# Optimization experiments

Hardware: AMD Instinct MI355X
Metric: run time of the kernel (lower is better)

## Reference

```python
import jax, jax.numpy as jnp
import numpy as np

EMBED_DIM = 1024
HEAD_SIZE = 64
N_HEAD = 16
N_QUERY_GROUPS = 4
SEQ_LEN = 2048
BATCH = 8


def setup_inputs() -> dict:
    key = jax.random.key(0)
    ks = jax.random.split(key, 7)
    s = 1.0 / np.sqrt(EMBED_DIM)
    x = jax.random.normal(ks[0], (BATCH, SEQ_LEN, EMBED_DIM), dtype=jnp.float32)
    Wq = jax.random.uniform(ks[1], (EMBED_DIM, N_HEAD * HEAD_SIZE), jnp.float32, -s, s)
    bq = jax.random.uniform(ks[2], (N_HEAD * HEAD_SIZE,), jnp.float32, -s, s)
    Wk = jax.random.uniform(ks[3], (EMBED_DIM, N_QUERY_GROUPS * HEAD_SIZE), jnp.float32, -s, s)
    bk = jax.random.uniform(ks[4], (N_QUERY_GROUPS * HEAD_SIZE,), jnp.float32, -s, s)
    Wv = jax.random.uniform(ks[5], (EMBED_DIM, N_QUERY_GROUPS * HEAD_SIZE), jnp.float32, -s, s)
    bv = jax.random.uniform(ks[6], (N_QUERY_GROUPS * HEAD_SIZE,), jnp.float32, -s, s)
    return {"x": x, "Wq": Wq, "bq": bq, "Wk": Wk, "bk": bk, "Wv": Wv, "bv": bv}


def reference(x, Wq, bq, Wk, bk, Wv, bv):
    B, T, _ = x.shape
    rep = N_HEAD // N_QUERY_GROUPS  # queries per group
    Q = x @ Wq + bq  # (B, T, H*hs)
    # GQA: torch .repeat tiles the group-block [g0..g3, g0..g3, ...]
    K = (x @ Wk + bk).reshape(B, T, N_QUERY_GROUPS, HEAD_SIZE)
    K = jnp.tile(K, (1, 1, rep, 1)).reshape(B, T, N_HEAD * HEAD_SIZE)
    V = (x @ Wv + bv).reshape(B, T, N_QUERY_GROUPS, HEAD_SIZE)
    V = jnp.tile(V, (1, 1, rep, 1)).reshape(B, T, N_HEAD * HEAD_SIZE)
    # flattened-head scores: contract over full H*hs dim (as in source)
    att = jnp.einsum('btd,bsd->bts', Q, K)  # (B, T, T)
    causal = jnp.triu(jnp.ones((T, T), dtype=bool), k=1)
    mask = jnp.where(causal, jnp.float32(-jnp.inf), jnp.float32(0.0))[None, None]  # (1,1,T,T)
    att = att + mask  # broadcasts to (1, B, T, T), matching torch semantics
    att = jax.nn.softmax(att, axis=-1) / jnp.sqrt(jnp.float32(HEAD_SIZE))  # post-hoc scale, as in source
    out = jnp.einsum('xbts,bsd->xbtd', att, V)  # (1, B, T, H*hs)
    return out
```

## Files before the change

### kernel.cpp

```cpp
#include <hip/hip_runtime.h>
#include <float.h>
#include <stdint.h>

#define T_ 2048
#define DG 256

typedef _Float16 half8 __attribute__((ext_vector_type(8)));
typedef _Float16 half4v __attribute__((ext_vector_type(4)));
typedef __fp16 fp16x2 __attribute__((ext_vector_type(2)));
typedef float f32x4 __attribute__((ext_vector_type(4)));
typedef float f32x16 __attribute__((ext_vector_type(16)));
typedef unsigned uint2v __attribute__((ext_vector_type(2)));

#define PSTRIDE 8256

__device__ __forceinline__ void gload16(const void* g, void* l) {
  __builtin_amdgcn_global_load_lds(
      (const __attribute__((address_space(1))) unsigned int*)g,
      (__attribute__((address_space(3))) unsigned int*)l, 16, 0, 0);
}
#define WAIT_VMC(N)  do { asm volatile("s_waitcnt vmcnt(" #N ")" ::: "memory"); __builtin_amdgcn_sched_barrier(0); } while (0)
#define WAIT_LGKM0() do { asm volatile("s_waitcnt lgkmcnt(0)" ::: "memory"); __builtin_amdgcn_sched_barrier(0); } while (0)

__device__ __forceinline__ float cross32(float x, int g) {
  unsigned u = __builtin_bit_cast(unsigned, x);
  uint2v r = __builtin_amdgcn_permlane32_swap(u, u, false, false);
  return __builtin_bit_cast(float, g ? r[0] : r[1]);
}

__global__ __launch_bounds__(256) void prep_w(
    const float* __restrict__ Wq, const float* __restrict__ bq,
    const float* __restrict__ Wk, const float* __restrict__ bk,
    const float* __restrict__ Wv, const float* __restrict__ bv,
    _Float16* __restrict__ Wt, float* __restrict__ bcat) {
  for (int idx = blockIdx.x * 256 + threadIdx.x; idx < 786432; idx += 768 * 256) {
    int n = idx >> 10, k = idx & 1023;
    float v;
    if (n < 256)      v = Wq[k * 1024 + n] + Wq[k * 1024 + n + 256]
                        + Wq[k * 1024 + n + 512] + Wq[k * 1024 + n + 768];
    else if (n < 512) v = Wk[k * 256 + n - 256];
    else              v = Wv[k * 256 + n - 512];
    Wt[idx] = (_Float16)v;
    if (k == 0) {
      float bb;
      if (n < 256)      bb = bq[n] + bq[n + 256] + bq[n + 512] + bq[n + 768];
      else if (n < 512) bb = bk[n - 256];
      else              bb = bv[n - 512];
      bcat[n] = bb;
    }
  }
}

__global__ __launch_bounds__(256) void qkv_gemm(
    const float* __restrict__ x, const _Float16* __restrict__ Wt,
    const float* __restrict__ bcat,
    _Float16* __restrict__ Qh, _Float16* __restrict__ Kh, _Float16* __restrict__ Vf) {
  __shared__ __align__(16) uint8_t smem[65536];
  const int tid = threadIdx.x;
  const int w = tid >> 6, l = tid & 63;
  const int wr = w >> 1, wc = w & 1;
  const int lr = l & 15, lk = l >> 4;
  const int id = blockIdx.x;
  const int xcd = id & 7, s = id >> 3;
  const int m0 = (xcd + 8 * (s / 3)) * 128;
  const int by = s % 3;
  const int n0 = by * 256;

  f32x4 acc[4][8] = {};

  auto stage = [&](int k0, int buf) {
    uint8_t* Ab = smem + buf * 32768;
    uint8_t* Bb = Ab + 16384;
#pragma unroll
    for (int i = 0; i < 4; ++i) {
      int si = i * 256 + tid;
      int row = si >> 3, p = si & 7;
      gload16(x + (size_t)(m0 + row) * 1024 + k0 + ((p ^ (row & 7)) << 2), Ab + si * 16);
    }
#pragma unroll
    for (int i = 0; i < 4; ++i) {
      int si = i * 256 + tid;
      int row = si >> 2, p = si & 3;
      gload16(Wt + (size_t)(n0 + row) * 1024 + k0 + ((p ^ (row & 3)) << 3), Bb + si * 16);
    }
  };

  stage(0, 0);
  __syncthreads();

  for (int kt = 0; kt < 32; ++kt) {
    int cur = kt & 1;
    if (kt < 31) stage((kt + 1) * 32, cur ^ 1);
    const uint8_t* Ab = smem + cur * 32768;
    const uint8_t* Bb = Ab + 16384;
    half8 af[4], bf[8];
#pragma unroll
    for (int mi = 0; mi < 4; ++mi) {
      int row = wr * 64 + mi * 16 + lr;
      const float* pa = (const float*)(Ab + row * 128);
      f32x4 a0 = *(const f32x4*)(pa + ((((lk << 1))     ^ (row & 7)) << 2));
      f32x4 a1 = *(const f32x4*)(pa + ((((lk << 1) | 1) ^ (row & 7)) << 2));
      half8 h;
#pragma unroll
      for (int j = 0; j < 4; ++j) { h[j] = (_Float16)a0[j]; h[j + 4] = (_Float16)a1[j]; }
      af[mi] = h;
    }
#pragma unroll
    for (int ni = 0; ni < 8; ++ni) {
      int row = wc * 128 + ni * 16 + lr;
      bf[ni] = *(const half8*)(Bb + row * 64 + ((lk ^ (row & 3)) << 4));
    }
#pragma unroll
    for (int mi = 0; mi < 4; ++mi)
#pragma unroll
      for (int ni = 0; ni < 8; ++ni)
        acc[mi][ni] = __builtin_amdgcn_mfma_f32_16x16x32_f16(af[mi], bf[ni], acc[mi][ni], 0, 0, 0);
    __syncthreads();
  }

#pragma unroll
  for (int mi = 0; mi < 4; ++mi) {
#pragma unroll
    for (int ni = 0; ni < 8; ++ni) {
      int nl = wc * 128 + ni * 16 + lr;
      int mg = m0 + wr * 64 + mi * 16 + lk * 4;
      float bias = bcat[n0 + nl];
      if (by == 0) {
#pragma unroll
        for (int r = 0; r < 4; ++r)
          Qh[(size_t)(mg + r) * DG + nl] = (_Float16)((acc[mi][ni][r] + bias) * 1.44269504f);
      } else if (by == 1) {
#pragma unroll
        for (int r = 0; r < 4; ++r)
          Kh[(size_t)(mg + r) * DG + nl] = (_Float16)(acc[mi][ni][r] + bias);
      } else {
        int dt = nl >> 5, lnv = nl & 31;
        int bb = mg >> 11, t0 = mg & 2047;
        int st = t0 >> 5, sp = t0 & 31;
        int hs = sp >> 4, gg = (sp >> 3) & 1, j0 = sp & 7;
        size_t idx = (size_t)(((bb * 64 + st) * 8 + dt) * 2 + hs) * 512
                   + (gg * 32 + lnv) * 8 + j0;
        half4v h;
#pragma unroll
        for (int r = 0; r < 4; ++r) h[r] = (_Float16)(acc[mi][ni][r] + bias);
        *(half4v*)(Vf + idx) = h;
      }
    }
  }
}

__global__ __launch_bounds__(256, 3) void attn_main(
    const _Float16* __restrict__ Qg, const _Float16* __restrict__ Kg,
    const _Float16* __restrict__ Vf, float* __restrict__ out,
    float* __restrict__ partials) {
  __shared__ __align__(16) uint8_t smem[53248];
  const int tid = threadIdx.x;
  const int wv = tid >> 6;
  const int l  = tid & 63;
  const int g  = l >> 5;
  const int ln = l & 31;
  const int id = blockIdx.x;
  const int b  = id & 7;
  const int u  = id >> 3;
  int tt, c, nc;
  if (u < 64) { tt = 63 - (u >> 1); c = u & 1; nc = 2; }
  else        { tt = 95 - u;        c = 0;     nc = 1; }
  const int h  = (tt + 1) >> 1;
  const int lo = (nc == 2 && c == 1) ? h : 0;
  const int hi = (nc == 2 && c == 0) ? h : tt + 1;
  const int q0 = tt * 32;

  const _Float16* Kb  = Kg + (size_t)b * T_ * DG;
  const _Float16* Vfb = Vf + (size_t)b * 524288;
  float* Sx = (float*)(smem + 32768);

  const _Float16* Qrow = Qg + ((size_t)(b * T_ + q0 + ln)) * DG + wv * 64 + 8 * g;
  half8 qf[4];
#pragma unroll
  for (int j = 0; j < 4; ++j) qf[j] = *(const half8*)(Qrow + j * 16);

  f32x16 o0 = {}, o1 = {};
  float m_r = -1e30f, l_r = 0.0f;

  auto stageK = [&](int s0, int buf) {
    uint8_t* Kl = smem + buf * 16384;
#pragma unroll
    for (int i = 0; i < 4; ++i) {
      int si = i * 256 + tid;
      int row = si >> 5, part = si & 31;
      gload16(Kb + (size_t)(s0 + row) * DG + ((part ^ (row & 7)) << 3), Kl + si * 16);
    }
  };

  stageK(lo * 32, 0);
  WAIT_VMC(0);
  __builtin_amdgcn_s_barrier();

  for (int kt = lo; kt < hi; ++kt) {
    int cur = (kt - lo) & 1;
    const int dt0 = 2 * wv;
    half8 va0 = *(const half8*)(Vfb + (size_t)((kt * 8 + dt0) * 2 + 0) * 512 + l * 8);
    half8 va1 = *(const half8*)(Vfb + (size_t)((kt * 8 + dt0) * 2 + 1) * 512 + l * 8);
    half8 vb0 = *(const half8*)(Vfb + (size_t)((kt * 8 + dt0 + 1) * 2 + 0) * 512 + l * 8);
    half8 vb1 = *(const half8*)(Vfb + (size_t)((kt * 8 + dt0 + 1) * 2 + 1) * 512 + l * 8);

    const uint8_t* Klds = smem + cur * 16384;
    const int xr = (ln & 7) << 4;
    f32x16 s_acc = {};
    __builtin_amdgcn_s_setprio(1);
#pragma unroll
    for (int j = 0; j < 4; ++j) {
      half8 kf = *(const half8*)(Klds + ln * 512 + ((((4 * wv + j) * 32) + 16 * g) ^ xr));
      s_acc = __builtin_amdgcn_mfma_f32_32x32x16_f16(kf, qf[j], s_acc, 0, 0, 0);
    }
    __builtin_amdgcn_s_setprio(0);

    {
      float* myrow = Sx + (wv * 64 + l) * 20;
#pragma unroll
      for (int i = 0; i < 4; ++i)
        *(f32x4*)(myrow + 4 * i) = *(((const f32x4*)&s_acc) + i);
    }
    if (kt + 1 < hi) stageK((kt + 1) * 32, cur ^ 1);
    WAIT_LGKM0();
    __builtin_amdgcn_s_barrier();

    f32x4 sv[4];
#pragma unroll
    for (int i = 0; i < 4; ++i) sv[i] = *(((const f32x4*)&s_acc) + i);
#pragma unroll
    for (int wo = 0; wo < 4; ++wo) {
      if (wo == wv) continue;
      const float* prow = Sx + (wo * 64 + l) * 20;
#pragma unroll
      for (int i = 0; i < 4; ++i) sv[i] += *(const f32x4*)(prow + 4 * i);
    }
    float s[16];
#pragma unroll
    for (int r = 0; r < 16; ++r) s[r] = sv[r >> 2][r & 3];

    if (kt == tt) {
#pragma unroll
      for (int r = 0; r < 16; ++r) {
        int srow = (r & 3) + 8 * (r >> 2) + 4 * g;
        if (srow > ln) s[r] = -1e30f;
      }
    }
    float pmax = s[0];
#pragma unroll
    for (int r = 1; r < 16; ++r) pmax = fmaxf(pmax, s[r]);
    pmax = fmaxf(pmax, cross32(pmax, g));
    if (!__all(pmax <= m_r + 8.0f)) {
      float mnew = fmaxf(m_r, pmax);
      float sc = __builtin_amdgcn_exp2f(m_r - mnew);
      l_r *= sc;
#pragma unroll
      for (int r = 0; r < 16; ++r) { o0[r] *= sc; o1[r] *= sc; }
      m_r = mnew;
    }
    float p[16]; float psum = 0.0f;
#pragma unroll
    for (int r = 0; r < 16; ++r) { p[r] = __builtin_amdgcn_exp2f(s[r] - m_r); psum += p[r]; }
    l_r += psum + cross32(psum, g);

    unsigned ph[8];
#pragma unroll
    for (int i = 0; i < 8; ++i) {
      fp16x2 t2 = __builtin_amdgcn_cvt_pkrtz(p[2 * i], p[2 * i + 1]);
      ph[i] = __builtin_bit_cast(unsigned, t2);
    }
    union U { unsigned u[4]; half8 h; };
    U f0, f1;
    {
      uint2v r02 = __builtin_amdgcn_permlane32_swap(ph[0], ph[2], false, false);
      uint2v r13 = __builtin_amdgcn_permlane32_swap(ph[1], ph[3], false, false);
      uint2v r46 = __builtin_amdgcn_permlane32_swap(ph[4], ph[6], false, false);
      uint2v r57 = __builtin_amdgcn_permlane32_swap(ph[5], ph[7], false, false);
      f0.u[0] = r02[0]; f0.u[2] = r02[1];
      f0.u[1] = r13[0]; f0.u[3] = r13[1];
      f1.u[0] = r46[0]; f1.u[2] = r46[1];
      f1.u[1] = r57[0]; f1.u[3] = r57[1];
    }

    __builtin_amdgcn_s_setprio(1);
    o0 = __builtin_amdgcn_mfma_f32_32x32x16_f16(va0, f0.h, o0, 0, 0, 0);
    o0 = __builtin_amdgcn_mfma_f32_32x32x16_f16(va1, f1.h, o0, 0, 0, 0);
    o1 = __builtin_amdgcn_mfma_f32_32x32x16_f16(vb0, f0.h, o1, 0, 0, 0);
    o1 = __builtin_amdgcn_mfma_f32_32x32x16_f16(vb1, f1.h, o1, 0, 0, 0);
    __builtin_amdgcn_s_setprio(0);

    WAIT_VMC(0);
    __builtin_amdgcn_s_barrier();
  }

  float* chunk = (float*)(smem + wv * 4352);
  if (nc == 1) {
    float inv = 1.0f / (l_r * 8.0f);
    float* ob = out + ((size_t)(b * T_ + q0)) * 1024;
#pragma unroll
    for (int dtl = 0; dtl < 2; ++dtl) {
      const f32x16& oo = dtl ? o1 : o0;
      WAIT_LGKM0();
#pragma unroll
      for (int r = 0; r < 16; ++r) {
        int dl = (r & 3) + 8 * (r >> 2) + 4 * g;
        chunk[ln * 33 + dl] = oo[r] * inv;
      }
      WAIT_LGKM0();
#pragma unroll
      for (int rr = 0; rr < 2; ++rr) {
        int qq = (l >> 2) + 16 * rr;
        int cp = (l & 3) * 8;
        float vv[8];
#pragma unroll
        for (int jj = 0; jj < 8; ++jj) vv[jj] = chunk[qq * 33 + cp + jj];
        float4 w0 = make_float4(vv[0], vv[1], vv[2], vv[3]);
        float4 w1 = make_float4(vv[4], vv[5], vv[6], vv[7]);
        float* orow = ob + (size_t)qq * 1024 + (2 * wv + dtl) * 32 + cp;
#pragma unroll
        for (int rep = 0; rep < 4; ++rep) {
          *(float4*)(orow + rep * 256)     = w0;
          *(float4*)(orow + rep * 256 + 4) = w1;
        }
      }
    }
  } else {
    float* P = partials + (size_t)((b * 32 + (tt - 32)) * 2 + c) * PSTRIDE;
#pragma unroll
    for (int dtl = 0; dtl < 2; ++dtl) {
      const f32x16& oo = dtl ? o1 : o0;
      WAIT_LGKM0();
#pragma unroll
      for (int r = 0; r < 16; ++r) {
        int dl = (r & 3) + 8 * (r >> 2) + 4 * g;
        chunk[ln * 33 + dl] = oo[r];
      }
      WAIT_LGKM0();
#pragma unroll
      for (int rr = 0; rr < 2; ++rr) {
        int qq = (l >> 2) + 16 * rr;
        int cp = (l & 3) * 8;
        float vv[8];
#pragma unroll
        for (int jj = 0; jj < 8; ++jj) vv[jj] = chunk[qq * 33 + cp + jj];
        float* prow = P + qq * 256 + (2 * wv + dtl) * 32 + cp;
        *(float4*)prow       = make_float4(vv[0], vv[1], vv[2], vv[3]);
        *(float4*)(prow + 4) = make_float4(vv[4], vv[5], vv[6], vv[7]);
      }
    }
    if (wv == 0 && l < 32) { P[8192 + l] = m_r; P[8224 + l] = l_r; }
  }
}

__global__ __launch_bounds__(256) void attn_merge(
    const float* __restrict__ partials, float* __restrict__ out) {
  const int id = blockIdx.x;
  const int b = id & 7, tt = 32 + (id >> 3);
  const float* P0 = partials + (size_t)((b * 32 + (tt - 32)) * 2) * PSTRIDE;
  const float* P1 = P0 + PSTRIDE;
  const int tid = threadIdx.x;
  const int row = tid >> 3, cb = tid & 7;
  float m0 = P0[8192 + row], l0v = P0[8224 + row];
  float m1 = P1[8192 + row], l1v = P1[8224 + row];
  float M   = fmaxf(m0, m1);
  float sc0 = __builtin_amdgcn_exp2f(m0 - M);
  float sc1 = __builtin_amdgcn_exp2f(m1 - M);
  float inv = 1.0f / ((l0v * sc0 + l1v * sc1) * 8.0f);
  const float4* r0 = (const float4*)(P0 + row * 256 + cb * 32);
  const float4* r1 = (const float4*)(P1 + row * 256 + cb * 32);
  float* orow = out + ((size_t)(b * T_ + tt * 32 + row)) * 1024 + cb * 32;
#pragma unroll
  for (int j = 0; j < 8; ++j) {
    float4 a = r0[j], bb = r1[j];
    float4 v;
    v.x = (a.x * sc0 + bb.x * sc1) * inv;
    v.y = (a.y * sc0 + bb.y * sc1) * inv;
    v.z = (a.z * sc0 + bb.z * sc1) * inv;
    v.w = (a.w * sc0 + bb.w * sc1) * inv;
#pragma unroll
    for (int rep = 0; rep < 4; ++rep)
      *(float4*)(orow + rep * 256 + j * 4) = v;
  }
}

extern "C" void kernel_launch(void* const* d_in, const int* in_sizes, int n_in,
                              void* d_out, int out_size, void* d_ws, size_t ws_size,
                              hipStream_t stream) {
  const float* x  = (const float*)d_in[0];
  const float* Wq = (const float*)d_in[1];
  const float* bq = (const float*)d_in[2];
  const float* Wk = (const float*)d_in[3];
  const float* bk = (const float*)d_in[4];
  const float* Wv = (const float*)d_in[5];
  const float* bv = (const float*)d_in[6];
  float* out = (float*)d_out;
  char* ws = (char*)d_ws;
  _Float16* Wt   = (_Float16*)ws;
  float*    bcat = (float*)(ws + 0x180000);
  _Float16* Qh   = (_Float16*)(ws + 0x181000);
  _Float16* Kh   = Qh + (size_t)16384 * 256;
  _Float16* Vf   = Kh + (size_t)16384 * 256;
  float* partials = (float*)(Vf + (size_t)16384 * 256);

  prep_w<<<768, 256, 0, stream>>>(Wq, bq, Wk, bk, Wv, bv, Wt, bcat);
  qkv_gemm<<<384, 256, 0, stream>>>(x, Wt, bcat, Qh, Kh, Vf);
  attn_main<<<768, 256, 0, stream>>>(Qh, Kh, Vf, out, partials);
  attn_merge<<<256, 256, 0, stream>>>(partials, out);
}
```

Baseline: 164.9 us.

## Pre-convert x to fp16, pre-swizzle K into MFMA fragments, rebalance attention split

Adds a separate kernel that converts x to fp16, so the QKV GEMM stages fp16 A tiles with half the shared memory and is launched on a 2D grid with narrower 128-column tiles. K is written through shared memory into a fragment-ready layout, which lets attention load K directly from global memory instead of staging it in LDS. Attention work is split more finely (1 to 4 chunks per query tile, 1280 blocks, occupancy hint raised to 4), and partial outputs are stored in fp16. This trades an extra conversion pass and fp16 partial precision for less LDS traffic and better load balance across blocks.

```diff
diff --git a/kernel.cpp b/kernel.cpp
--- a/kernel.cpp
+++ b/kernel.cpp
@@ -12,14 +12,11 @@
 typedef float f32x16 __attribute__((ext_vector_type(16)));
 typedef unsigned uint2v __attribute__((ext_vector_type(2)));
 
-#define PSTRIDE 8256
-
 __device__ __forceinline__ void gload16(const void* g, void* l) {
   __builtin_amdgcn_global_load_lds(
       (const __attribute__((address_space(1))) unsigned int*)g,
       (__attribute__((address_space(3))) unsigned int*)l, 16, 0, 0);
 }
-#define WAIT_VMC(N)  do { asm volatile("s_waitcnt vmcnt(" #N ")" ::: "memory"); __builtin_amdgcn_sched_barrier(0); } while (0)
 #define WAIT_LGKM0() do { asm volatile("s_waitcnt lgkmcnt(0)" ::: "memory"); __builtin_amdgcn_sched_barrier(0); } while (0)
 
 __device__ __forceinline__ float cross32(float x, int g) {
@@ -51,37 +48,47 @@
   }
 }
 
+__global__ __launch_bounds__(256) void xcvt(const float* __restrict__ x,
+                                            _Float16* __restrict__ xh) {
+  size_t i = (size_t)blockIdx.x * 256 + threadIdx.x;
+  const float4* s = (const float4*)x + i * 2;
+  float4 a = s[0], b = s[1];
+  half8 h;
+  h[0] = (_Float16)a.x; h[1] = (_Float16)a.y; h[2] = (_Float16)a.z; h[3] = (_Float16)a.w;
+  h[4] = (_Float16)b.x; h[5] = (_Float16)b.y; h[6] = (_Float16)b.z; h[7] = (_Float16)b.w;
+  *(half8*)(xh + i * 8) = h;
+}
+
 __global__ __launch_bounds__(256) void qkv_gemm(
-    const float* __restrict__ x, const _Float16* __restrict__ Wt,
+    const _Float16* __restrict__ xh, const _Float16* __restrict__ Wt,
     const float* __restrict__ bcat,
-    _Float16* __restrict__ Qh, _Float16* __restrict__ Kh, _Float16* __restrict__ Vf) {
-  __shared__ __align__(16) uint8_t smem[65536];
+    _Float16* __restrict__ Qh, _Float16* __restrict__ Kf, _Float16* __restrict__ Vf) {
+  __shared__ __align__(16) uint8_t smem[32768];
   const int tid = threadIdx.x;
   const int w = tid >> 6, l = tid & 63;
   const int wr = w >> 1, wc = w & 1;
   const int lr = l & 15, lk = l >> 4;
-  const int id = blockIdx.x;
-  const int xcd = id & 7, s = id >> 3;
-  const int m0 = (xcd + 8 * (s / 3)) * 128;
-  const int by = s % 3;
-  const int n0 = by * 256;
-
-  f32x4 acc[4][8] = {};
+  const int m0 = blockIdx.x * 128;
+  const int by = blockIdx.y >> 1;
+  const int nh = blockIdx.y & 1;
+
+  f32x4 acc[4][4] = {};
 
   auto stage = [&](int k0, int buf) {
-    uint8_t* Ab = smem + buf * 32768;
-    uint8_t* Bb = Ab + 16384;
-#pragma unroll
-    for (int i = 0; i < 4; ++i) {
-      int si = i * 256 + tid;
-      int row = si >> 3, p = si & 7;
-      gload16(x + (size_t)(m0 + row) * 1024 + k0 + ((p ^ (row & 7)) << 2), Ab + si * 16);
-    }
-#pragma unroll
-    for (int i = 0; i < 4; ++i) {
+    uint8_t* Ab = smem + buf * 16384;
+    uint8_t* Bb = Ab + 8192;
+#pragma unroll
+    for (int i = 0; i < 2; ++i) {
       int si = i * 256 + tid;
       int row = si >> 2, p = si & 3;
-      gload16(Wt + (size_t)(n0 + row) * 1024 + k0 + ((p ^ (row & 3)) << 3), Bb + si * 16);
+      gload16(xh + (size_t)(m0 + row) * 1024 + k0 + ((p ^ (row & 3)) << 3), Ab + si * 16);
+    }
+#pragma unroll
+    for (int i = 0; i < 2; ++i) {
+      int si = i * 256 + tid;
+      int row = si >> 2, p = si & 3;
+      gload16(Wt + (size_t)(by * 256 + nh * 128 + row) * 1024 + k0 + ((p ^ (row & 3)) << 3),
+              Bb + si * 16);
     }
   };
 
@@ -91,49 +98,47 @@
   for (int kt = 0; kt < 32; ++kt) {
     int cur = kt & 1;
     if (kt < 31) stage((kt + 1) * 32, cur ^ 1);
-    const uint8_t* Ab = smem + cur * 32768;
-    const uint8_t* Bb = Ab + 16384;
-    half8 af[4], bf[8];
+    const uint8_t* Ab = smem + cur * 16384;
+    const uint8_t* Bb = Ab + 8192;
+    half8 af[4], bf[4];
 #pragma unroll
     for (int mi = 0; mi < 4; ++mi) {
       int row = wr * 64 + mi * 16 + lr;
-      const float* pa = (const float*)(Ab + row * 128);
-      f32x4 a0 = *(const f32x4*)(pa + ((((lk << 1))     ^ (row & 7)) << 2));
-      f32x4 a1 = *(const f32x4*)(pa + ((((lk << 1) | 1) ^ (row & 7)) << 2));
-      half8 h;
-#pragma unroll
-      for (int j = 0; j < 4; ++j) { h[j] = (_Float16)a0[j]; h[j + 4] = (_Float16)a1[j]; }
-      af[mi] = h;
-    }
-#pragma unroll
-    for (int ni = 0; ni < 8; ++ni) {
-      int row = wc * 128 + ni * 16 + lr;
+      af[mi] = *(const half8*)(Ab + row * 64 + ((lk ^ (row & 3)) << 4));
+    }
+#pragma unroll
+    for (int ni = 0; ni < 4; ++ni) {
+      int row = wc * 64 + ni * 16 + lr;
       bf[ni] = *(const half8*)(Bb + row * 64 + ((lk ^ (row & 3)) << 4));
     }
 #pragma unroll
     for (int mi = 0; mi < 4; ++mi)
 #pragma unroll
-      for (int ni = 0; ni < 8; ++ni)
+      for (int ni = 0; ni < 4; ++ni)
         acc[mi][ni] = __builtin_amdgcn_mfma_f32_16x16x32_f16(af[mi], bf[ni], acc[mi][ni], 0, 0, 0);
     __syncthreads();
   }
 
-#pragma unroll
-  for (int mi = 0; mi < 4; ++mi) {
-#pragma unroll
-    for (int ni = 0; ni < 8; ++ni) {
-      int nl = wc * 128 + ni * 16 + lr;
-      int mg = m0 + wr * 64 + mi * 16 + lk * 4;
-      float bias = bcat[n0 + nl];
-      if (by == 0) {
+  if (by == 0) {
+#pragma unroll
+    for (int mi = 0; mi < 4; ++mi)
+#pragma unroll
+      for (int ni = 0; ni < 4; ++ni) {
+        int nl = nh * 128 + wc * 64 + ni * 16 + lr;
+        int mg = m0 + wr * 64 + mi * 16 + lk * 4;
+        float bias = bcat[nl];
 #pragma unroll
         for (int r = 0; r < 4; ++r)
           Qh[(size_t)(mg + r) * DG + nl] = (_Float16)((acc[mi][ni][r] + bias) * 1.44269504f);
-      } else if (by == 1) {
-#pragma unroll
-        for (int r = 0; r < 4; ++r)
-          Kh[(size_t)(mg + r) * DG + nl] = (_Float16)(acc[mi][ni][r] + bias);
-      } else {
+      }
+  } else if (by == 2) {
+#pragma unroll
+    for (int mi = 0; mi < 4; ++mi)
+#pragma unroll
+      for (int ni = 0; ni < 4; ++ni) {
+        int nl = nh * 128 + wc * 64 + ni * 16 + lr;
+        int mg = m0 + wr * 64 + mi * 16 + lk * 4;
+        float bias = bcat[512 + nl];
         int dt = nl >> 5, lnv = nl & 31;
         int bb = mg >> 11, t0 = mg & 2047;
         int st = t0 >> 5, sp = t0 & 31;
@@ -145,15 +150,41 @@
         for (int r = 0; r < 4; ++r) h[r] = (_Float16)(acc[mi][ni][r] + bias);
         *(half4v*)(Vf + idx) = h;
       }
-    }
-  }
-}
-
-__global__ __launch_bounds__(256, 3) void attn_main(
-    const _Float16* __restrict__ Qg, const _Float16* __restrict__ Kg,
+  } else {
+#pragma unroll
+    for (int mi = 0; mi < 4; ++mi)
+#pragma unroll
+      for (int ni = 0; ni < 4; ++ni) {
+        int dl = wc * 64 + ni * 16 + lr;
+        float bias = bcat[256 + nh * 128 + dl];
+#pragma unroll
+        for (int r = 0; r < 4; ++r) {
+          int t = wr * 64 + mi * 16 + lk * 4 + r;
+          *(_Float16*)(smem + t * 256 + ((dl * 2) ^ ((t & 7) << 4))) =
+              (_Float16)(acc[mi][ni][r] + bias);
+        }
+      }
+    __syncthreads();
+#pragma unroll
+    for (int i = 0; i < 8; ++i) {
+      int p = i * 256 + tid;
+      int ln = p & 31, g = (p >> 5) & 1, cl = (p >> 6) & 7, st = p >> 9;
+      int t = st * 32 + ln;
+      int d0 = cl * 16 + g * 8;
+      half8 v = *(const half8*)(smem + t * 256 + ((d0 * 2) ^ ((t & 7) << 4)));
+      int tg = m0 + t;
+      int bb = tg >> 11, stg = (tg & 2047) >> 5;
+      int cc = nh * 8 + cl;
+      *(half8*)(Kf + ((size_t)(((bb * 64 + stg) * 16 + cc) * 2 + g) * 32 + ln) * 8) = v;
+    }
+  }
+}
+
+__global__ __launch_bounds__(256, 4) void attn_main(
+    const _Float16* __restrict__ Qg, const _Float16* __restrict__ Kf,
     const _Float16* __restrict__ Vf, float* __restrict__ out,
-    float* __restrict__ partials) {
-  __shared__ __align__(16) uint8_t smem[53248];
+    _Float16* __restrict__ PO, float* __restrict__ ML) {
+  __shared__ float Sx[5120];
   const int tid = threadIdx.x;
   const int wv = tid >> 6;
   const int l  = tid & 63;
@@ -162,17 +193,18 @@
   const int id = blockIdx.x;
   const int b  = id & 7;
   const int u  = id >> 3;
-  int tt, c, nc;
-  if (u < 64) { tt = 63 - (u >> 1); c = u & 1; nc = 2; }
-  else        { tt = 95 - u;        c = 0;     nc = 1; }
-  const int h  = (tt + 1) >> 1;
-  const int lo = (nc == 2 && c == 1) ? h : 0;
-  const int hi = (nc == 2 && c == 0) ? h : tt + 1;
-  const int q0 = tt * 32;
-
-  const _Float16* Kb  = Kg + (size_t)b * T_ * DG;
+  int tt, nc, c;
+  if (u < 16)      { tt = u;                  nc = 1; c = 0; }
+  else if (u < 48) { tt = 16 + ((u - 16) >> 1); nc = 2; c = (u - 16) & 1; }
+  else if (u < 96) { tt = 32 + (u - 48) / 3;  nc = 3; c = (u - 48) % 3; }
+  else             { tt = 48 + ((u - 96) >> 2); nc = 4; c = (u - 96) & 3; }
+  const int len = (tt + nc) / nc;
+  const int lo  = c * len;
+  const int hi  = min(lo + len, tt + 1);
+  const int q0  = tt * 32;
+
+  const _Float16* Kfb = Kf + (size_t)b * 524288;
   const _Float16* Vfb = Vf + (size_t)b * 524288;
-  float* Sx = (float*)(smem + 32768);
 
   const _Float16* Qrow = Qg + ((size_t)(b * T_ + q0 + ln)) * DG + wv * 64 + 8 * g;
   half8 qf[4];
@@ -182,37 +214,24 @@
   f32x16 o0 = {}, o1 = {};
   float m_r = -1e30f, l_r = 0.0f;
 
-  auto stageK = [&](int s0, int buf) {
-    uint8_t* Kl = smem + buf * 16384;
-#pragma unroll
-    for (int i = 0; i < 4; ++i) {
-      int si = i * 256 + tid;
-      int row = si >> 5, part = si & 31;
-      gload16(Kb + (size_t)(s0 + row) * DG + ((part ^ (row & 7)) << 3), Kl + si * 16);
-    }
-  };
-
-  stageK(lo * 32, 0);
-  WAIT_VMC(0);
-  __builtin_amdgcn_s_barrier();
-
   for (int kt = lo; kt < hi; ++kt) {
-    int cur = (kt - lo) & 1;
-    const int dt0 = 2 * wv;
-    half8 va0 = *(const half8*)(Vfb + (size_t)((kt * 8 + dt0) * 2 + 0) * 512 + l * 8);
-    half8 va1 = *(const half8*)(Vfb + (size_t)((kt * 8 + dt0) * 2 + 1) * 512 + l * 8);
-    half8 vb0 = *(const half8*)(Vfb + (size_t)((kt * 8 + dt0 + 1) * 2 + 0) * 512 + l * 8);
-    half8 vb1 = *(const half8*)(Vfb + (size_t)((kt * 8 + dt0 + 1) * 2 + 1) * 512 + l * 8);
-
-    const uint8_t* Klds = smem + cur * 16384;
-    const int xr = (ln & 7) << 4;
+    const _Float16* kbase = Kfb + (size_t)(kt * 16 + 4 * wv) * 512 + l * 8;
+    half8 kf0 = *(const half8*)(kbase);
+    half8 kf1 = *(const half8*)(kbase + 512);
+    half8 kf2 = *(const half8*)(kbase + 1024);
+    half8 kf3 = *(const half8*)(kbase + 1536);
+    const _Float16* vbase = Vfb + (size_t)(kt * 8 + 2 * wv) * 1024 + l * 8;
+    half8 va0 = *(const half8*)(vbase);
+    half8 va1 = *(const half8*)(vbase + 512);
+    half8 vb0 = *(const half8*)(vbase + 1024);
+    half8 vb1 = *(const half8*)(vbase + 1536);
+
     f32x16 s_acc = {};
     __builtin_amdgcn_s_setprio(1);
-#pragma unroll
-    for (int j = 0; j < 4; ++j) {
-      half8 kf = *(const half8*)(Klds + ln * 512 + ((((4 * wv + j) * 32) + 16 * g) ^ xr));
-      s_acc = __builtin_amdgcn_mfma_f32_32x32x16_f16(kf, qf[j], s_acc, 0, 0, 0);
-    }
+    s_acc = __builtin_amdgcn_mfma_f32_32x32x16_f16(kf0, qf[0], s_acc, 0, 0, 0);
+    s_acc = __builtin_amdgcn_mfma_f32_32x32x16_f16(kf1, qf[1], s_acc, 0, 0, 0);
+    s_acc = __builtin_amdgcn_mfma_f32_32x32x16_f16(kf2, qf[2], s_acc, 0, 0, 0);
+    s_acc = __builtin_amdgcn_mfma_f32_32x32x16_f16(kf3, qf[3], s_acc, 0, 0, 0);
     __builtin_amdgcn_s_setprio(0);
 
     {
@@ -221,7 +240,6 @@
       for (int i = 0; i < 4; ++i)
         *(f32x4*)(myrow + 4 * i) = *(((const f32x4*)&s_acc) + i);
     }
-    if (kt + 1 < hi) stageK((kt + 1) * 32, cur ^ 1);
     WAIT_LGKM0();
     __builtin_amdgcn_s_barrier();
 
@@ -289,11 +307,10 @@
     o1 = __builtin_amdgcn_mfma_f32_32x32x16_f16(vb1, f1.h, o1, 0, 0, 0);
     __builtin_amdgcn_s_setprio(0);
 
-    WAIT_VMC(0);
     __builtin_amdgcn_s_barrier();
   }
 
-  float* chunk = (float*)(smem + wv * 4352);
+  float* chunk = Sx + wv * 1280;
   if (nc == 1) {
     float inv = 1.0f / (l_r * 8.0f);
     float* ob = out + ((size_t)(b * T_ + q0)) * 1024;
@@ -325,7 +342,10 @@
       }
     }
   } else {
-    float* P = partials + (size_t)((b * 32 + (tt - 32)) * 2 + c) * PSTRIDE;
+    int ti = tt - 16;
+    int off = (ti < 16) ? ti * 2 : (ti < 32) ? 32 + (ti - 16) * 3 : 80 + (ti - 32) * 4;
+    int slot = b * 144 + off + c;
+    _Float16* P = PO + (size_t)slot * 8192;
 #pragma unroll
     for (int dtl = 0; dtl < 2; ++dtl) {
       const f32x16& oo = dtl ? o1 : o0;
@@ -340,46 +360,68 @@
       for (int rr = 0; rr < 2; ++rr) {
         int qq = (l >> 2) + 16 * rr;
         int cp = (l & 3) * 8;
-        float vv[8];
-#pragma unroll
-        for (int jj = 0; jj < 8; ++jj) vv[jj] = chunk[qq * 33 + cp + jj];
-        float* prow = P + qq * 256 + (2 * wv + dtl) * 32 + cp;
-        *(float4*)prow       = make_float4(vv[0], vv[1], vv[2], vv[3]);
-        *(float4*)(prow + 4) = make_float4(vv[4], vv[5], vv[6], vv[7]);
-      }
-    }
-    if (wv == 0 && l < 32) { P[8192 + l] = m_r; P[8224 + l] = l_r; }
+        half8 hv;
+#pragma unroll
+        for (int jj = 0; jj < 8; ++jj) hv[jj] = (_Float16)chunk[qq * 33 + cp + jj];
+        *(half8*)(P + qq * 256 + (2 * wv + dtl) * 32 + cp) = hv;
+      }
+    }
+    if (wv == 0 && l < 32) {
+      ML[(size_t)slot * 64 + l]      = m_r;
+      ML[(size_t)slot * 64 + 32 + l] = l_r;
+    }
   }
 }
 
 __global__ __launch_bounds__(256) void attn_merge(
-    const float* __restrict__ partials, float* __restrict__ out) {
+    const _Float16* __restrict__ PO, const float* __restrict__ ML,
+    float* __restrict__ out) {
   const int id = blockIdx.x;
-  const int b = id & 7, tt = 32 + (id >> 3);
-  const float* P0 = partials + (size_t)((b * 32 + (tt - 32)) * 2) * PSTRIDE;
-  const float* P1 = P0 + PSTRIDE;
+  const int b = id & 7, ti = id >> 3;
+  const int tt = 16 + ti;
+  const int nc = (ti < 16) ? 2 : (ti < 32) ? 3 : 4;
+  const int off = (ti < 16) ? ti * 2 : (ti < 32) ? 32 + (ti - 16) * 3 : 80 + (ti - 32) * 4;
+  const int slot0 = b * 144 + off;
   const int tid = threadIdx.x;
   const int row = tid >> 3, cb = tid & 7;
-  float m0 = P0[8192 + row], l0v = P0[8224 + row];
-  float m1 = P1[8192 + row], l1v = P1[8224 + row];
-  float M   = fmaxf(m0, m1);
-  float sc0 = __builtin_amdgcn_exp2f(m0 - M);
-  float sc1 = __builtin_amdgcn_exp2f(m1 - M);
-  float inv = 1.0f / ((l0v * sc0 + l1v * sc1) * 8.0f);
-  const float4* r0 = (const float4*)(P0 + row * 256 + cb * 32);
-  const float4* r1 = (const float4*)(P1 + row * 256 + cb * 32);
+
+  float mj[4], lj[4];
+  float M = -1e30f;
+#pragma unroll
+  for (int j = 0; j < 4; ++j)
+    if (j < nc) {
+      mj[j] = ML[(size_t)(slot0 + j) * 64 + row];
+      lj[j] = ML[(size_t)(slot0 + j) * 64 + 32 + row];
+      M = fmaxf(M, mj[j]);
+    }
+  float sc[4], lsum = 0.0f;
+#pragma unroll
+  for (int j = 0; j < 4; ++j)
+    if (j < nc) { sc[j] = __builtin_amdgcn_exp2f(mj[j] - M); lsum += lj[j] * sc[j]; }
+  float inv = 1.0f / (lsum * 8.0f);
+
+  float acc[32] = {};
+#pragma unroll
+  for (int j = 0; j < 4; ++j)
+    if (j < nc) {
+      const _Float16* P = PO + (size_t)(slot0 + j) * 8192 + row * 256 + cb * 32;
+      float s = sc[j];
+#pragma unroll
+      for (int q = 0; q < 4; ++q) {
+        half8 h = *(const half8*)(P + q * 8);
+#pragma unroll
+        for (int e = 0; e < 8; ++e) acc[q * 8 + e] += s * (float)h[e];
+      }
+    }
   float* orow = out + ((size_t)(b * T_ + tt * 32 + row)) * 1024 + cb * 32;
 #pragma unroll
-  for (int j = 0; j < 8; ++j) {
-    float4 a = r0[j], bb = r1[j];
+  for (int q = 0; q < 8; ++q) {
     float4 v;
-    v.x = (a.x * sc0 + bb.x * sc1) * inv;
-    v.y = (a.y * sc0 + bb.y * sc1) * inv;
-    v.z = (a.z * sc0 + bb.z * sc1) * inv;
-    v.w = (a.w * sc0 + bb.w * sc1) * inv;
+    v.x = acc[q * 4 + 0] * inv; v.y = acc[q * 4 + 1] * inv;
+    v.z = acc[q * 4 + 2] * inv; v.w = acc[q * 4 + 3] * inv;
 #pragma unroll
     for (int rep = 0; rep < 4; ++rep)
-      *(float4*)(orow + rep * 256 + j * 4) = v;
+      *(float4*)(orow + rep * 256 + q * 4) = v;
   }
 }
 
@@ -398,12 +440,15 @@
   _Float16* Wt   = (_Float16*)ws;
   float*    bcat = (float*)(ws + 0x180000);
   _Float16* Qh   = (_Float16*)(ws + 0x181000);
-  _Float16* Kh   = Qh + (size_t)16384 * 256;
-  _Float16* Vf   = Kh + (size_t)16384 * 256;
-  float* partials = (float*)(Vf + (size_t)16384 * 256);
+  _Float16* Kf   = (_Float16*)(ws + 0x981000);
+  _Float16* Vf   = (_Float16*)(ws + 0x1181000);
+  _Float16* xh   = (_Float16*)(ws + 0x1981000);
+  _Float16* PO   = (_Float16*)(ws + 0x1981000);
+  float*    ML   = (float*)(ws + 0x1981000 + 0x1200000);
 
   prep_w<<<768, 256, 0, stream>>>(Wq, bq, Wk, bk, Wv, bv, Wt, bcat);
-  qkv_gemm<<<384, 256, 0, stream>>>(x, Wt, bcat, Qh, Kh, Vf);
-  attn_main<<<768, 256, 0, stream>>>(Qh, Kh, Vf, out, partials);
-  attn_merge<<<256, 256, 0, stream>>>(partials, out);
-}
+  xcvt<<<8192, 256, 0, stream>>>(x, xh);
+  qkv_gemm<<<dim3(128, 6), 256, 0, stream>>>(xh, Wt, bcat, Qh, Kf, Vf);
+  attn_main<<<1280, 256, 0, stream>>>(Qh, Kf, Vf, out, PO, ML);
+  attn_merge<<<384, 256, 0, stream>>>(PO, ML, out);
+}
```

New measurement: 156.8 us. -4.9%, faster.
